# Optimization experiments

Hardware: AMD Instinct MI355X
Metric: run time of the kernel (lower is better)

Reference implementation:

```python
import jax
import jax.numpy as jnp
from jax import lax
import numpy as np

N_NODES = 1_000_000
DEGREE = 31            # neighbors per agent -> group_size = DEGREE + 1
GROUP = DEGREE + 1
THRESHOLD = 16         # CRD threshold M = group_size / 2
COST = 0.25            # CRD cooperation cost c


def setup_inputs() -> dict:
    key = jax.random.key(0)
    k1, k2 = jax.random.split(key)
    gains = jax.random.normal(k1, (N_NODES,), dtype=jnp.float32)
    neighbors = jax.random.randint(k2, (N_NODES, DEGREE), 0, N_NODES, dtype=jnp.int64)
    return {"gains": gains, "neighbors": neighbors}


def reference(gains, neighbors):
    # sigmoid cooperation prob per agent, then neighbor gather -> [N, GROUP]
    p = jax.nn.sigmoid(gains)                       # [N]
    group_p = jnp.concatenate([p[:, None], p[neighbors]], axis=1)  # [N, GROUP]

    # Poisson-Binomial PMF via DP convolution over group members.
    # dp[n, k] = P(k cooperators among members processed so far)
    n = group_p.shape[0]
    dp0 = jnp.zeros((n, GROUP + 1), dtype=group_p.dtype).at[:, 0].set(1.0)

    def step(dp, pj):  # pj: [N] coop prob of one group member
        pj = pj[:, None]
        shifted = jnp.pad(dp[:, :-1], ((0, 0), (1, 0)))  # dp shifted by one success
        return dp * (1.0 - pj) + shifted * pj, None

    dp, _ = lax.scan(step, dp0, group_p.T)          # scan over GROUP members

    prob_above = dp[:, THRESHOLD:].sum(axis=1)      # P(count >= THRESHOLD), [N]
    acum_loss = jnp.sum(prob_above - COST * p)
    return -acum_loss
```

## Files before the change

### kernel.cpp

```cpp
#include <hip/hip_runtime.h>

constexpr int DEG   = 31;
constexpr int NEV   = 32;
constexpr int TH    = 16;
constexpr int BLK   = 256;

__global__ void zero_out_kernel(float* out) {
    if (threadIdx.x == 0) out[0] = 0.0f;
}

__device__ __forceinline__ float fast_sigmoid(float x) {
    return 1.0f / (1.0f + __expf(-x));
}

__global__ __launch_bounds__(BLK)
void pgl_kernel(const float* __restrict__ gains,
                const int*   __restrict__ nbr,
                float*       __restrict__ out,
                int n) {
    __shared__ int s_idx[BLK * DEG];
    __shared__ float s_red[BLK / 64];

    const int tid        = threadIdx.x;
    const int blockStart = blockIdx.x * BLK;

    const int rows  = min(BLK, n - blockStart);
    const int elems = rows * DEG;
    const int base  = blockStart * DEG;

    const int4* nb4 = (const int4*)(nbr + base);
    int4*       s4  = (int4*)s_idx;
    const int nvec  = elems >> 2;
    for (int v = tid; v < nvec; v += BLK) s4[v] = nb4[v];
    for (int e = (nvec << 2) + tid; e < elems; e += BLK) s_idx[e] = nbr[base + e];
    __syncthreads();

    float local = 0.0f;
    const int i = blockStart + tid;
    if (i < n) {
        const int* row = s_idx + tid * DEG;

        float dp[TH];
        dp[0] = 1.0f;
        #pragma unroll
        for (int k = 1; k < TH; ++k) dp[k] = 0.0f;
        float over = 0.0f;

        const float p0 = fast_sigmoid(gains[i]);

        #pragma unroll
        for (int j = 0; j < NEV; ++j) {
            float pj;
            if (j == 0) {
                pj = p0;
            } else {
                const int idx = row[j - 1];
                pj = fast_sigmoid(gains[idx]);
            }
            if (j >= TH - 1) over = fmaf(dp[TH - 1], pj, over);
            const int kmax = (j + 1 < TH - 1) ? (j + 1) : (TH - 1);
            #pragma unroll
            for (int k = kmax; k >= 1; --k)
                dp[k] = fmaf(pj, dp[k - 1] - dp[k], dp[k]);
            dp[0] = fmaf(-pj, dp[0], dp[0]);
        }
        local = fmaf(0.25f, p0, -over);
    }

    #pragma unroll
    for (int off = 32; off > 0; off >>= 1)
        local += __shfl_down(local, off, 64);
    if ((tid & 63) == 0) s_red[tid >> 6] = local;
    __syncthreads();
    if (tid == 0) {
        float s = 0.0f;
        #pragma unroll
        for (int w = 0; w < BLK / 64; ++w) s += s_red[w];
        atomicAdd(out, s);
    }
}

extern "C" void kernel_launch(void* const* d_in, const int* in_sizes, int n_in,
                              void* d_out, int out_size, void* d_ws, size_t ws_size,
                              hipStream_t stream) {
    const float* gains = (const float*)d_in[0];
    const int*   nbr   = (const int*)d_in[1];
    float*       out   = (float*)d_out;
    const int n = in_sizes[0];

    zero_out_kernel<<<1, 64, 0, stream>>>(out);
    const int grid = (n + BLK - 1) / BLK;
    pgl_kernel<<<grid, BLK, 0, stream>>>(gains, nbr, out, n);
}
```

Baseline: 308.6 us.

## Precompute fp16 sigmoid table and stream it through LDS in chunks

Adds a pre-pass that computes sigmoid(gains) once and stores it as a half-precision table in workspace. The main kernel then uses 1024-thread blocks and streams the whole 2 MB table through LDS in 16 chunks of 64K entries. Each thread picks up its neighbours' probabilities from LDS when the chunk matching an index's high bits is resident. This replaces random global gathers and repeated exp evaluations with sequential table streaming and LDS lookups. In exchange every block reads the entire table, which adds heavy global traffic and many barriers, and fp16 probabilities lose precision; a direct fallback kernel runs when workspace is too small.

```diff
diff --git a/kernel.cpp b/kernel.cpp
--- a/kernel.cpp
+++ b/kernel.cpp
@@ -1,45 +1,94 @@
 #include <hip/hip_runtime.h>
+#include <hip/hip_fp16.h>
 
 constexpr int DEG   = 31;
-constexpr int NEV   = 32;
 constexpr int TH    = 16;
-constexpr int BLK   = 256;
+constexpr int BLK   = 1024;
+constexpr int CHUNK = 65536;
+constexpr int NCHNK = 16;
+constexpr int TBL   = NCHNK * CHUNK;
+
+__device__ __forceinline__ float fast_sigmoid(float x) {
+    return 1.0f / (1.0f + __expf(-x));
+}
 
 __global__ void zero_out_kernel(float* out) {
     if (threadIdx.x == 0) out[0] = 0.0f;
 }
 
-__device__ __forceinline__ float fast_sigmoid(float x) {
-    return 1.0f / (1.0f + __expf(-x));
+__global__ __launch_bounds__(256)
+void build_table_kernel(const float* __restrict__ gains,
+                        __half* __restrict__ tbl, int n) {
+    const int i = blockIdx.x * 256 + threadIdx.x;
+    if (i < TBL) {
+        float p = 0.0f;
+        if (i < n) p = fast_sigmoid(gains[i]);
+        tbl[i] = __float2half_rn(p);
+    }
 }
 
 __global__ __launch_bounds__(BLK)
-void pgl_kernel(const float* __restrict__ gains,
-                const int*   __restrict__ nbr,
-                float*       __restrict__ out,
-                int n) {
-    __shared__ int s_idx[BLK * DEG];
+void pgl_lds_kernel(const float* __restrict__ gains,
+                    const int*   __restrict__ nbr,
+                    const __half* __restrict__ tbl,
+                    float*       __restrict__ out, int n) {
+    __shared__ __align__(16) unsigned char lds_raw[CHUNK * 2];
     __shared__ float s_red[BLK / 64];
 
     const int tid        = threadIdx.x;
     const int blockStart = blockIdx.x * BLK;
+    const int i          = blockStart + tid;
 
     const int rows  = min(BLK, n - blockStart);
     const int elems = rows * DEG;
     const int base  = blockStart * DEG;
-
-    const int4* nb4 = (const int4*)(nbr + base);
-    int4*       s4  = (int4*)s_idx;
-    const int nvec  = elems >> 2;
-    for (int v = tid; v < nvec; v += BLK) s4[v] = nb4[v];
-    for (int e = (nvec << 2) + tid; e < elems; e += BLK) s_idx[e] = nbr[base + e];
+    {
+        const int4* nb4 = (const int4*)(nbr + base);
+        int4*       s4  = (int4*)lds_raw;
+        int*        s1  = (int*)lds_raw;
+        const int nvec = elems >> 2;
+        for (int v = tid; v < nvec; v += BLK) s4[v] = nb4[v];
+        for (int e = (nvec << 2) + tid; e < elems; e += BLK) s1[e] = nbr[base + e];
+    }
     __syncthreads();
 
+    unsigned idx[DEG];
+    if (i < n) {
+        const int* sidx = (const int*)lds_raw;
+        #pragma unroll
+        for (int j = 0; j < DEG; ++j) idx[j] = (unsigned)sidx[tid * DEG + j];
+    } else {
+        #pragma unroll
+        for (int j = 0; j < DEG; ++j) idx[j] = 0u;
+    }
+    __syncthreads();
+
+    __half pv[DEG];
+    #pragma unroll
+    for (int j = 0; j < DEG; ++j) pv[j] = __half(0.0f);
+
+    const int4* tbl4 = (const int4*)tbl;
+    for (int c = 0; c < NCHNK; ++c) {
+        int4* c4 = (int4*)lds_raw;
+        const int cbase = c * (CHUNK / 8);
+        #pragma unroll
+        for (int t = 0; t < (CHUNK / 8) / BLK; ++t) {
+            const int v = t * BLK + tid;
+            c4[v] = tbl4[cbase + v];
+        }
+        __syncthreads();
+
+        const __half* ch = (const __half*)lds_raw;
+        #pragma unroll
+        for (int j = 0; j < DEG; ++j) {
+            if ((idx[j] >> 16) == (unsigned)c)
+                pv[j] = ch[idx[j] & 0xFFFFu];
+        }
+        __syncthreads();
+    }
+
     float local = 0.0f;
-    const int i = blockStart + tid;
     if (i < n) {
-        const int* row = s_idx + tid * DEG;
-
         float dp[TH];
         dp[0] = 1.0f;
         #pragma unroll
@@ -49,14 +98,8 @@
         const float p0 = fast_sigmoid(gains[i]);
 
         #pragma unroll
-        for (int j = 0; j < NEV; ++j) {
-            float pj;
-            if (j == 0) {
-                pj = p0;
-            } else {
-                const int idx = row[j - 1];
-                pj = fast_sigmoid(gains[idx]);
-            }
+        for (int j = 0; j <= DEG; ++j) {
+            const float pj = (j == 0) ? p0 : __half2float(pv[j - 1]);
             if (j >= TH - 1) over = fmaf(dp[TH - 1], pj, over);
             const int kmax = (j + 1 < TH - 1) ? (j + 1) : (TH - 1);
             #pragma unroll
@@ -68,14 +111,65 @@
     }
 
     #pragma unroll
-    for (int off = 32; off > 0; off >>= 1)
-        local += __shfl_down(local, off, 64);
+    for (int o = 32; o > 0; o >>= 1) local += __shfl_down(local, o, 64);
     if ((tid & 63) == 0) s_red[tid >> 6] = local;
     __syncthreads();
     if (tid == 0) {
         float s = 0.0f;
         #pragma unroll
         for (int w = 0; w < BLK / 64; ++w) s += s_red[w];
+        atomicAdd(out, s);
+    }
+}
+
+constexpr int FBLK = 128;
+__global__ __launch_bounds__(FBLK)
+void pgl_direct_kernel(const float* __restrict__ gains,
+                       const int*   __restrict__ nbr,
+                       float*       __restrict__ out, int n) {
+    __shared__ int s_idx[FBLK * DEG];
+    __shared__ float s_red[FBLK / 64];
+    const int tid = threadIdx.x;
+    const int blockStart = blockIdx.x * FBLK;
+    const int rows  = min(FBLK, n - blockStart);
+    const int elems = rows * DEG;
+    const int base  = blockStart * DEG;
+    const int4* nb4 = (const int4*)(nbr + base);
+    int4* s4 = (int4*)s_idx;
+    const int nvec = elems >> 2;
+    for (int v = tid; v < nvec; v += FBLK) s4[v] = nb4[v];
+    for (int e = (nvec << 2) + tid; e < elems; e += FBLK) s_idx[e] = nbr[base + e];
+    __syncthreads();
+    float local = 0.0f;
+    const int i = blockStart + tid;
+    if (i < n) {
+        const int* row = s_idx + tid * DEG;
+        float dp[TH];
+        dp[0] = 1.0f;
+        #pragma unroll
+        for (int k = 1; k < TH; ++k) dp[k] = 0.0f;
+        float over = 0.0f;
+        const float p0 = fast_sigmoid(gains[i]);
+        #pragma unroll
+        for (int j = 0; j <= DEG; ++j) {
+            const float pj = (j == 0) ? p0 : fast_sigmoid(gains[row[j - 1]]);
+            if (j >= TH - 1) over = fmaf(dp[TH - 1], pj, over);
+            const int kmax = (j + 1 < TH - 1) ? (j + 1) : (TH - 1);
+            #pragma unroll
+            for (int k = kmax; k >= 1; --k)
+                dp[k] = fmaf(pj, dp[k - 1] - dp[k], dp[k]);
+            dp[0] = fmaf(-pj, dp[0], dp[0]);
+        }
+        local = fmaf(0.25f, p0, -over);
+    }
+    #pragma unroll
+    for (int o = 32; o > 0; o >>= 1) local += __shfl_down(local, o, 64);
+    if ((tid & 63) == 0) s_red[tid >> 6] = local;
+    __syncthreads();
+    if (tid == 0) {
+        float s = 0.0f;
+        #pragma unroll
+        for (int w = 0; w < FBLK / 64; ++w) s += s_red[w];
         atomicAdd(out, s);
     }
 }
@@ -89,6 +183,14 @@
     const int n = in_sizes[0];
 
     zero_out_kernel<<<1, 64, 0, stream>>>(out);
-    const int grid = (n + BLK - 1) / BLK;
-    pgl_kernel<<<grid, BLK, 0, stream>>>(gains, nbr, out, n);
+
+    if (ws_size >= (size_t)TBL * sizeof(__half)) {
+        __half* tbl = (__half*)d_ws;
+        build_table_kernel<<<(TBL + 255) / 256, 256, 0, stream>>>(gains, tbl, n);
+        const int grid = (n + BLK - 1) / BLK;
+        pgl_lds_kernel<<<grid, BLK, 0, stream>>>(gains, nbr, tbl, out, n);
+    } else {
+        const int grid = (n + FBLK - 1) / FBLK;
+        pgl_direct_kernel<<<grid, FBLK, 0, stream>>>(gains, nbr, out, n);
+    }
 }
```

New measurement: 399.1 us. 29.3% more time.
